# Kernel tuning notes

Hardware: AMD Instinct MI355X
Metric: run time of the kernel (lower is better)

## Reference

```python
import jax, jax.numpy as jnp
import numpy as np

B, S, IN_DIM = 2048, 65, 256
H, L = 8, 256


def setup_inputs() -> dict:
    key = jax.random.key(0)
    ks = jax.random.split(key, 8)
    return {
        "x": jax.random.normal(ks[0], (B, S, IN_DIM), dtype=jnp.float32),
        "Wq": jax.random.normal(ks[1], (H, IN_DIM, L), dtype=jnp.float32),
        "Wk": jax.random.normal(ks[2], (H, IN_DIM, L), dtype=jnp.float32),
        "Wv": jax.random.normal(ks[3], (H, IN_DIM, L), dtype=jnp.float32),
        "W": jax.random.normal(ks[4], (H, L, 1), dtype=jnp.float32),
        "O": jax.random.normal(ks[5], (H * L, IN_DIM), dtype=jnp.float32),
        "P": jax.random.normal(ks[6], (S - 1, IN_DIM), dtype=jnp.float32),
        "bias": jax.random.normal(ks[7], (H,), dtype=jnp.float32),
    }


def reference(x, Wq, Wk, Wv, W, O, P, bias):
    origin = x[:, 0, :]                       # [B, D]
    walk = x[:, 1:, :]                        # [B, S-1, D]
    origin_seq = origin[:, None, :] + P       # [B, S-1, D]

    # per-head sigmoid projections, vectorized over heads
    k = jax.nn.sigmoid(jnp.einsum('bsd,hdl->bhsl', origin_seq, Wk))
    q = jax.nn.sigmoid(jnp.einsum('bsd,hdl->bhsl', walk, Wq))
    v = jax.nn.sigmoid(jnp.einsum('bsd,hdl->bhsl', walk, Wv))

    edge = jnp.cos(k * q) + bias[None, :, None, None]       # [B,H,S-1,L]
    score = jnp.einsum('bhsl,hl->bhs', edge, W[..., 0])      # [B,H,S-1]
    score = jax.nn.softmax(score, axis=-1)
    res = jnp.einsum('bhs,bhsl->bhl', score, v)              # [B,H,L]
    res = res.reshape(res.shape[0], H * L)                   # concat heads
    out = jax.nn.sigmoid(res @ O)                            # [B, D]
    return jnp.concatenate([out, origin], axis=-1)           # [B, 2D]
```

## Files before the change

### kernel.cpp

```cpp
#include <hip/hip_runtime.h>
#include <math.h>

#define NB   2048
#define NSEQ 65
#define ND   256
#define NH   8
#define NL   256
#define NS   64
#define APAD 264

typedef _Float16 f16;
typedef _Float16 f16x4 __attribute__((ext_vector_type(4)));
typedef _Float16 f16x8 __attribute__((ext_vector_type(8)));
typedef float    f32x4 __attribute__((ext_vector_type(4)));

__device__ __forceinline__ float sigmoidf_(float x) {
    return __builtin_amdgcn_rcpf(1.0f + __expf(-x));
}

__global__ __launch_bounds__(256) void xh_kernel(const float* __restrict__ x,
                                                 f16* __restrict__ xh) {
    int flat8 = blockIdx.x * 256 + threadIdx.x;
    int b  = flat8 >> 11;
    int rm = flat8 & 2047;
    int s  = rm >> 5;
    int k8 = rm & 31;
    const float* src = x + (size_t)b * (NSEQ * ND) + (1 + s) * ND + k8 * 8;
    float4 v0 = *(const float4*)(src);
    float4 v1 = *(const float4*)(src + 4);
    f16x8 o = {(f16)v0.x, (f16)v0.y, (f16)v0.z, (f16)v0.w,
               (f16)v1.x, (f16)v1.y, (f16)v1.z, (f16)v1.w};
    *(f16x8*)(xh + (size_t)b * 16384 + s * 256 + k8 * 8) = o;
}

__global__ __launch_bounds__(256) void wh_kernel(const float* __restrict__ Wq,
                                                 const float* __restrict__ Wv,
                                                 const float* __restrict__ Wk,
                                                 f16* __restrict__ wh) {
    int hm = blockIdx.x >> 4;
    int h  = hm / 3, m = hm % 3;
    int n  = ((blockIdx.x & 15) << 4) + (threadIdx.x >> 4);
    int kc = (threadIdx.x & 15) << 4;
    const float* src = (m == 0 ? Wq : (m == 1 ? Wv : Wk)) + h * (ND * NL);
    f16x8 t0, t1;
    #pragma unroll
    for (int j = 0; j < 8; ++j) t0[j] = (f16)src[(kc + j) * NL + n];
    #pragma unroll
    for (int j = 0; j < 8; ++j) t1[j] = (f16)src[(kc + 8 + j) * NL + n];
    f16* dst = wh + ((size_t)(hm * 256 + n)) * 256 + kc;
    *(f16x8*)dst       = t0;
    *(f16x8*)(dst + 8) = t1;
}

__global__ __launch_bounds__(256) void ot_kernel(const float* __restrict__ O,
                                                 f16* __restrict__ OT) {
    int n = blockIdx.x;
    int t = threadIdx.x;
    f16x8 v;
    #pragma unroll
    for (int j = 0; j < 8; ++j) v[j] = (f16)O[(size_t)(t * 8 + j) * 256 + n];
    *(f16x8*)(OT + (size_t)n * 2048 + t * 8) = v;
}

__global__ __launch_bounds__(256) void pkt_kernel(const float* __restrict__ P,
                                                  const float* __restrict__ Wk,
                                                  float* __restrict__ PKT) {
    int h = blockIdx.x >> 6;
    int s = blockIdx.x & 63;
    int t = threadIdx.x;
    __shared__ float p_s[ND];
    p_s[t] = P[s * ND + t];
    __syncthreads();
    const float* wk = Wk + h * (ND * NL) + t;
    float acc = 0.f;
    #pragma unroll 8
    for (int d = 0; d < ND; ++d) acc = fmaf(p_s[d], wk[d * NL], acc);
    PKT[((size_t)h * NL + t) * NS + s] = acc;
}

__global__ __launch_bounds__(256) void ok_gemm(const float* __restrict__ x,
                                               const f16*   __restrict__ wh,
                                               float* __restrict__ OK) {
    int mblk = blockIdx.x >> 4;
    int nblk = blockIdx.x & 15;
    int b0 = mblk * 64;
    int h  = nblk >> 1;
    int l0 = (nblk & 1) * 128;
    int t = threadIdx.x;
    int w = t >> 6, lane = t & 63, c = lane & 15, g = lane >> 4;

    __shared__ f16 Ao[64 * APAD];
    #pragma unroll
    for (int it = 0; it < 16; ++it) {
        int idx4 = it * 256 + t;
        int s = idx4 >> 6, kq = idx4 & 63;
        float4 v = *(const float4*)(x + (size_t)(b0 + s) * (NSEQ * ND) + kq * 4);
        *(f16x4*)(&Ao[s * APAD + kq * 4]) = (f16x4){(f16)v.x, (f16)v.y, (f16)v.z, (f16)v.w};
    }
    __syncthreads();

    f32x4 acc[4][2];
    #pragma unroll
    for (int mt = 0; mt < 4; ++mt)
        #pragma unroll
        for (int nt = 0; nt < 2; ++nt) acc[mt][nt] = (f32x4){0.f, 0.f, 0.f, 0.f};

    const f16* bb = wh + ((size_t)((h * 3 + 2) * 256 + l0 + w * 32 + c)) * 256;
    #pragma unroll 2
    for (int kk = 0; kk < 8; ++kk) {
        int k0 = kk * 32 + g * 8;
        f16x8 af[4];
        #pragma unroll
        for (int mt = 0; mt < 4; ++mt)
            af[mt] = *(const f16x8*)(&Ao[(mt * 16 + c) * APAD + k0]);
        #pragma unroll
        for (int nt = 0; nt < 2; ++nt) {
            f16x8 bf = *(const f16x8*)(bb + nt * 16 * 256 + k0);
            #pragma unroll
            for (int mt = 0; mt < 4; ++mt)
                acc[mt][nt] = __builtin_amdgcn_mfma_f32_16x16x32_f16(af[mt], bf, acc[mt][nt], 0, 0, 0);
        }
    }
    #pragma unroll
    for (int mt = 0; mt < 4; ++mt)
        #pragma unroll
        for (int nt = 0; nt < 2; ++nt)
            #pragma unroll
            for (int r = 0; r < 4; ++r)
                OK[((size_t)h * NB + b0 + mt * 16 + g * 4 + r) * NL + l0 + w * 32 + nt * 16 + c]
                    = acc[mt][nt][r];
}

__global__ __launch_bounds__(256, 2) void attn_mfma(
        const f16*   __restrict__ xh,
        const f16*   __restrict__ wh,
        const float* __restrict__ W,
        const float* __restrict__ PKT,
        const float* __restrict__ OK,
        f16* __restrict__ res) {
    int b = blockIdx.x;
    int t = threadIdx.x;
    int w    = t >> 6;
    int lane = t & 63;
    int c = lane & 15;
    int g = lane >> 4;

    f16x8 af[4][8];
    const f16* xb = xh + (size_t)b * 16384 + c * 256 + g * 8;
    #pragma unroll
    for (int mt = 0; mt < 4; ++mt)
        #pragma unroll
        for (int kk = 0; kk < 8; ++kk)
            af[mt][kk] = *(const f16x8*)(xb + mt * 16 * 256 + kk * 32);

    int rot  = b & 7;
    int hrot = (b >> 3) & 1;

    #pragma unroll
    for (int hh = 0; hh < 2; ++hh) {
        int h = w * 2 + ((hh + hrot) & 1);

        float part[4][4];
        #pragma unroll
        for (int mt = 0; mt < 4; ++mt)
            #pragma unroll
            for (int r = 0; r < 4; ++r) part[mt][r] = 0.f;

        for (int ci = 0; ci < 8; ++ci) {
            int ch = (ci + rot) & 7;
            f32x4 acc[4][2];
            #pragma unroll
            for (int mt = 0; mt < 4; ++mt)
                #pragma unroll
                for (int nt = 0; nt < 2; ++nt) acc[mt][nt] = (f32x4){0.f, 0.f, 0.f, 0.f};

            const f16* bq = wh + ((size_t)((h * 3 + 0) * 256 + ch * 32 + c)) * 256 + g * 8;
            #pragma unroll
            for (int kk = 0; kk < 8; ++kk) {
                #pragma unroll
                for (int nt = 0; nt < 2; ++nt) {
                    f16x8 bf = *(const f16x8*)(bq + nt * 16 * 256 + kk * 32);
                    #pragma unroll
                    for (int mt = 0; mt < 4; ++mt)
                        acc[mt][nt] = __builtin_amdgcn_mfma_f32_16x16x32_f16(af[mt][kk], bf, acc[mt][nt], 0, 0, 0);
                }
            }
            #pragma unroll
            for (int nt = 0; nt < 2; ++nt) {
                int l = ch * 32 + nt * 16 + c;
                float wl  = W[h * NL + l];
                float okv = OK[((size_t)h * NB + b) * NL + l];
                const float* pkcol = PKT + ((size_t)h * NL + l) * NS + g * 4;
                #pragma unroll
                for (int mt = 0; mt < 4; ++mt) {
                    float4 pk4 = *(const float4*)(pkcol + mt * 16);
                    float pks[4] = {pk4.x, pk4.y, pk4.z, pk4.w};
                    #pragma unroll
                    for (int r = 0; r < 4; ++r) {
                        float qs = sigmoidf_(acc[mt][nt][r]);
                        float ks = sigmoidf_(okv + pks[r]);
                        part[mt][r] = fmaf(__cosf(ks * qs), wl, part[mt][r]);
                    }
                }
            }
        }

        #pragma unroll
        for (int mt = 0; mt < 4; ++mt)
            #pragma unroll
            for (int r = 0; r < 4; ++r) {
                float v = part[mt][r];
                v += __shfl_xor(v, 1, 64);
                v += __shfl_xor(v, 2, 64);
                v += __shfl_xor(v, 4, 64);
                v += __shfl_xor(v, 8, 64);
                part[mt][r] = v;
            }
        float m = part[0][0];
        #pragma unroll
        for (int mt = 0; mt < 4; ++mt)
            #pragma unroll
            for (int r = 0; r < 4; ++r) m = fmaxf(m, part[mt][r]);
        m = fmaxf(m, __shfl_xor(m, 16, 64));
        m = fmaxf(m, __shfl_xor(m, 32, 64));
        float ssum = 0.f;
        #pragma unroll
        for (int mt = 0; mt < 4; ++mt)
            #pragma unroll
            for (int r = 0; r < 4; ++r) {
                float e = __expf(part[mt][r] - m);
                part[mt][r] = e;
                ssum += e;
            }
        ssum += __shfl_xor(ssum, 16, 64);
        ssum += __shfl_xor(ssum, 32, 64);
        float rinv = __builtin_amdgcn_rcpf(ssum);
        #pragma unroll
        for (int mt = 0; mt < 4; ++mt)
            #pragma unroll
            for (int r = 0; r < 4; ++r) part[mt][r] *= rinv;

        for (int ci = 0; ci < 8; ++ci) {
            int ch = (ci + rot) & 7;
            f32x4 acc[4][2];
            #pragma unroll
            for (int mt = 0; mt < 4; ++mt)
                #pragma unroll
                for (int nt = 0; nt < 2; ++nt) acc[mt][nt] = (f32x4){0.f, 0.f, 0.f, 0.f};

            const f16* bv = wh + ((size_t)((h * 3 + 1) * 256 + ch * 32 + c)) * 256 + g * 8;
            #pragma unroll
            for (int kk = 0; kk < 8; ++kk) {
                #pragma unroll
                for (int nt = 0; nt < 2; ++nt) {
                    f16x8 bf = *(const f16x8*)(bv + nt * 16 * 256 + kk * 32);
                    #pragma unroll
                    for (int mt = 0; mt < 4; ++mt)
                        acc[mt][nt] = __builtin_amdgcn_mfma_f32_16x16x32_f16(af[mt][kk], bf, acc[mt][nt], 0, 0, 0);
                }
            }
            #pragma unroll
            for (int nt = 0; nt < 2; ++nt) {
                float v = 0.f;
                #pragma unroll
                for (int mt = 0; mt < 4; ++mt)
                    #pragma unroll
                    for (int r = 0; r < 4; ++r)
                        v = fmaf(part[mt][r], sigmoidf_(acc[mt][nt][r]), v);
                v += __shfl_xor(v, 16, 64);
                v += __shfl_xor(v, 32, 64);
                if (g == 0)
                    res[(size_t)b * 2048 + h * NL + ch * 32 + nt * 16 + c] = (f16)v;
            }
        }
    }
}

__global__ __launch_bounds__(256) void out_gemm(
        const float* __restrict__ x,
        const f16*   __restrict__ res,
        const f16*   __restrict__ OT,
        float* __restrict__ out) {
    int mblk = blockIdx.x >> 1;
    int nblk = blockIdx.x & 1;
    int b0 = mblk * 32;
    int t  = threadIdx.x;
    int w    = t >> 6;
    int lane = t & 63;
    int c = lane & 15;
    int g = lane >> 4;

    __shared__ f16 Ao[32 * APAD];

    f32x4 acc[2][2];
    #pragma unroll
    for (int mt = 0; mt < 2; ++mt)
        #pragma unroll
        for (int nt = 0; nt < 2; ++nt) acc[mt][nt] = (f32x4){0.f, 0.f, 0.f, 0.f};

    for (int chunk = 0; chunk < 8; ++chunk) {
        int kbase = chunk * 256;
        __syncthreads();
        #pragma unroll
        for (int it = 0; it < 4; ++it) {
            int id  = it * 256 + t;
            int row = id >> 5;
            int kc  = (id & 31) << 3;
            *(f16x8*)(&Ao[row * APAD + kc]) =
                *(const f16x8*)(res + (size_t)(b0 + row) * 2048 + kbase + kc);
        }
        __syncthreads();
        #pragma unroll
        for (int kk = 0; kk < 8; ++kk) {
            int k0 = kk * 32 + g * 8;
            f16x8 af[2];
            #pragma unroll
            for (int mt = 0; mt < 2; ++mt)
                af[mt] = *(const f16x8*)(&Ao[(mt * 16 + c) * APAD + k0]);
            #pragma unroll
            for (int nt = 0; nt < 2; ++nt) {
                f16x8 bf = *(const f16x8*)(OT + (size_t)(nblk * 128 + w * 32 + nt * 16 + c) * 2048 + kbase + k0);
                #pragma unroll
                for (int mt = 0; mt < 2; ++mt)
                    acc[mt][nt] = __builtin_amdgcn_mfma_f32_16x16x32_f16(af[mt], bf, acc[mt][nt], 0, 0, 0);
            }
        }
    }
    #pragma unroll
    for (int mt = 0; mt < 2; ++mt)
        #pragma unroll
        for (int nt = 0; nt < 2; ++nt)
            #pragma unroll
            for (int r = 0; r < 4; ++r) {
                int row = mt * 16 + g * 4 + r;
                int col = nblk * 128 + w * 32 + nt * 16 + c;
                out[(size_t)(b0 + row) * 512 + col] = sigmoidf_(acc[mt][nt][r]);
            }
    if (nblk == 1) {
        for (int r2 = 0; r2 < 32; ++r2)
            out[(size_t)(b0 + r2) * 512 + 256 + t] = x[(size_t)(b0 + r2) * (NSEQ * ND) + t];
    }
}

extern "C" void kernel_launch(void* const* d_in, const int* in_sizes, int n_in,
                              void* d_out, int out_size, void* d_ws, size_t ws_size,
                              hipStream_t stream) {
    const float* x    = (const float*)d_in[0];
    const float* Wq   = (const float*)d_in[1];
    const float* Wk   = (const float*)d_in[2];
    const float* Wv   = (const float*)d_in[3];
    const float* W    = (const float*)d_in[4];
    const float* O    = (const float*)d_in[5];
    const float* P    = (const float*)d_in[6];
    float* out = (float*)d_out;

    char* wsb = (char*)d_ws;
    f16*   wh  = (f16*)wsb;
    f16*   OT  = (f16*)(wsb + 3145728);
    float* PKT = (float*)(wsb + 4194304);
    float* OK  = (float*)(wsb + 4718592);
    f16*   res = (f16*)(wsb + 21495808);
    f16*   xh  = (f16*)(wsb + 29884416);

    xh_kernel<<<16384, 256, 0, stream>>>(x, xh);
    wh_kernel<<<384, 256, 0, stream>>>(Wq, Wv, Wk, wh);
    ot_kernel<<<256, 256, 0, stream>>>(O, OT);
    pkt_kernel<<<NH * NS, 256, 0, stream>>>(P, Wk, PKT);
    ok_gemm<<<512, 256, 0, stream>>>(x, wh, OK);
    attn_mfma<<<NB, 256, 0, stream>>>(xh, wh, W, PKT, OK, res);
    out_gemm<<<128, 256, 0, stream>>>(x, res, OT, out);
}
```

Before: 917.3 us.

## Software-pipeline MFMA tiles with epilogue math and use native cosine

Restructures the per-head Q and V loops into 16 chunks of 16 columns, double-buffered in accumulators. Each chunk's MFMA work is issued while the sigmoid/cos/softmax-weighted epilogue of the previous chunk runs, and the first V chunk is prefetched before the softmax. It also replaces __cosf with the hardware cos instruction on pre-scaled input, and keeps the head loop rolled to limit register pressure. The aim is to overlap matrix-core latency with transcendental VALU work. The cost is more live accumulator registers and a possible occupancy or spill risk.

```diff
diff --git a/kernel.cpp b/kernel.cpp
--- a/kernel.cpp
+++ b/kernel.cpp
@@ -16,6 +16,9 @@
 
 __device__ __forceinline__ float sigmoidf_(float x) {
     return __builtin_amdgcn_rcpf(1.0f + __expf(-x));
+}
+__device__ __forceinline__ float cos01_(float x) {
+    return __builtin_amdgcn_cosf(x * 0.15915494309189535f);
 }
 
 __global__ __launch_bounds__(256) void xh_kernel(const float* __restrict__ x,
@@ -153,12 +156,17 @@
         for (int kk = 0; kk < 8; ++kk)
             af[mt][kk] = *(const f16x8*)(xb + mt * 16 * 256 + kk * 32);
 
-    int rot  = b & 7;
-    int hrot = (b >> 3) & 1;
-
-    #pragma unroll
+    int rot  = b & 15;
+    int hrot = (b >> 4) & 1;
+
+    #pragma unroll 1
     for (int hh = 0; hh < 2; ++hh) {
         int h = w * 2 + ((hh + hrot) & 1);
+        const f16* bqbase = wh + ((size_t)((h * 3 + 0) * 256 + c)) * 256 + g * 8;
+        const f16* bvbase = wh + ((size_t)((h * 3 + 1) * 256 + c)) * 256 + g * 8;
+        const float* Wp   = W + h * NL + c;
+        const float* OKp  = OK + ((size_t)h * NB + b) * NL + c;
+        const float* PKp  = PKT + ((size_t)h * NL + c) * NS + g * 4;
 
         float part[4][4];
         #pragma unroll
@@ -166,42 +174,55 @@
             #pragma unroll
             for (int r = 0; r < 4; ++r) part[mt][r] = 0.f;
 
-        for (int ci = 0; ci < 8; ++ci) {
-            int ch = (ci + rot) & 7;
-            f32x4 acc[4][2];
-            #pragma unroll
-            for (int mt = 0; mt < 4; ++mt)
-                #pragma unroll
-                for (int nt = 0; nt < 2; ++nt) acc[mt][nt] = (f32x4){0.f, 0.f, 0.f, 0.f};
-
-            const f16* bq = wh + ((size_t)((h * 3 + 0) * 256 + ch * 32 + c)) * 256 + g * 8;
-            #pragma unroll
-            for (int kk = 0; kk < 8; ++kk) {
-                #pragma unroll
-                for (int nt = 0; nt < 2; ++nt) {
-                    f16x8 bf = *(const f16x8*)(bq + nt * 16 * 256 + kk * 32);
+        f32x4 accP[2][4];
+
+        #pragma unroll
+        for (int ci = 0; ci <= 16; ++ci) {
+            int pi = ci & 1;
+            if (ci < 16) {
+                int ch = (ci + rot) & 15;
+                const f16* bq = bqbase + (size_t)(ch * 16) * 256;
+                #pragma unroll
+                for (int mt = 0; mt < 4; ++mt) accP[pi][mt] = (f32x4){0.f, 0.f, 0.f, 0.f};
+                #pragma unroll
+                for (int kk = 0; kk < 8; ++kk) {
+                    f16x8 bf = *(const f16x8*)(bq + kk * 32);
                     #pragma unroll
                     for (int mt = 0; mt < 4; ++mt)
-                        acc[mt][nt] = __builtin_amdgcn_mfma_f32_16x16x32_f16(af[mt][kk], bf, acc[mt][nt], 0, 0, 0);
+                        accP[pi][mt] = __builtin_amdgcn_mfma_f32_16x16x32_f16(af[mt][kk], bf, accP[pi][mt], 0, 0, 0);
                 }
             }
-            #pragma unroll
-            for (int nt = 0; nt < 2; ++nt) {
-                int l = ch * 32 + nt * 16 + c;
-                float wl  = W[h * NL + l];
-                float okv = OK[((size_t)h * NB + b) * NL + l];
-                const float* pkcol = PKT + ((size_t)h * NL + l) * NS + g * 4;
+            if (ci > 0) {
+                int qi = pi ^ 1;
+                int chp = (ci - 1 + rot) & 15;
+                int lo = chp * 16;
+                float wl  = Wp[lo];
+                float okv = OKp[lo];
+                const float* pkcol = PKp + (size_t)lo * NS;
                 #pragma unroll
                 for (int mt = 0; mt < 4; ++mt) {
                     float4 pk4 = *(const float4*)(pkcol + mt * 16);
                     float pks[4] = {pk4.x, pk4.y, pk4.z, pk4.w};
                     #pragma unroll
                     for (int r = 0; r < 4; ++r) {
-                        float qs = sigmoidf_(acc[mt][nt][r]);
+                        float qs = sigmoidf_(accP[qi][mt][r]);
                         float ks = sigmoidf_(okv + pks[r]);
-                        part[mt][r] = fmaf(__cosf(ks * qs), wl, part[mt][r]);
+                        part[mt][r] = fmaf(cos01_(ks * qs), wl, part[mt][r]);
                     }
                 }
+            }
+        }
+
+        {
+            const f16* bv = bvbase + (size_t)((rot & 15) * 16) * 256;
+            #pragma unroll
+            for (int mt = 0; mt < 4; ++mt) accP[0][mt] = (f32x4){0.f, 0.f, 0.f, 0.f};
+            #pragma unroll
+            for (int kk = 0; kk < 8; ++kk) {
+                f16x8 bf = *(const f16x8*)(bv + kk * 32);
+                #pragma unroll
+                for (int mt = 0; mt < 4; ++mt)
+                    accP[0][mt] = __builtin_amdgcn_mfma_f32_16x16x32_f16(af[mt][kk], bf, accP[0][mt], 0, 0, 0);
             }
         }
 
@@ -240,37 +261,35 @@
             #pragma unroll
             for (int r = 0; r < 4; ++r) part[mt][r] *= rinv;
 
-        for (int ci = 0; ci < 8; ++ci) {
-            int ch = (ci + rot) & 7;
-            f32x4 acc[4][2];
-            #pragma unroll
-            for (int mt = 0; mt < 4; ++mt)
-                #pragma unroll
-                for (int nt = 0; nt < 2; ++nt) acc[mt][nt] = (f32x4){0.f, 0.f, 0.f, 0.f};
-
-            const f16* bv = wh + ((size_t)((h * 3 + 1) * 256 + ch * 32 + c)) * 256 + g * 8;
-            #pragma unroll
-            for (int kk = 0; kk < 8; ++kk) {
-                #pragma unroll
-                for (int nt = 0; nt < 2; ++nt) {
-                    f16x8 bf = *(const f16x8*)(bv + nt * 16 * 256 + kk * 32);
+        #pragma unroll
+        for (int ci = 1; ci <= 16; ++ci) {
+            int pi = ci & 1;
+            if (ci < 16) {
+                int ch = (ci + rot) & 15;
+                const f16* bv = bvbase + (size_t)(ch * 16) * 256;
+                #pragma unroll
+                for (int mt = 0; mt < 4; ++mt) accP[pi][mt] = (f32x4){0.f, 0.f, 0.f, 0.f};
+                #pragma unroll
+                for (int kk = 0; kk < 8; ++kk) {
+                    f16x8 bf = *(const f16x8*)(bv + kk * 32);
                     #pragma unroll
                     for (int mt = 0; mt < 4; ++mt)
-                        acc[mt][nt] = __builtin_amdgcn_mfma_f32_16x16x32_f16(af[mt][kk], bf, acc[mt][nt], 0, 0, 0);
+                        accP[pi][mt] = __builtin_amdgcn_mfma_f32_16x16x32_f16(af[mt][kk], bf, accP[pi][mt], 0, 0, 0);
                 }
             }
-            #pragma unroll
-            for (int nt = 0; nt < 2; ++nt) {
+            {
+                int qi = pi ^ 1;
+                int chp = (ci - 1 + rot) & 15;
                 float v = 0.f;
                 #pragma unroll
                 for (int mt = 0; mt < 4; ++mt)
                     #pragma unroll
                     for (int r = 0; r < 4; ++r)
-                        v = fmaf(part[mt][r], sigmoidf_(acc[mt][nt][r]), v);
+                        v = fmaf(part[mt][r], sigmoidf_(accP[qi][mt][r]), v);
                 v += __shfl_xor(v, 16, 64);
                 v += __shfl_xor(v, 32, 64);
                 if (g == 0)
-                    res[(size_t)b * 2048 + h * NL + ch * 32 + nt * 16 + c] = (f16)v;
+                    res[(size_t)b * 2048 + h * NL + chp * 16 + c] = (f16)v;
             }
         }
     }
```

New measurement: 874.4 us. 4.7% less time.
